# Performance work log

Measured on AMD Instinct MI355X. Metric: run time of the kernel, lower is better.

Reference implementation:

```python
import math
import jax, jax.numpy as jnp
import numpy as np

B, K, D, R = 8192, 64, 128, 8
EPSILON = 1.0  # alpha_scale, used as diffusion epsilon


def setup_inputs() -> dict:
    key = jax.random.key(0)
    k1, k2, k3 = jax.random.split(key, 3)
    y = jax.random.normal(k1, (B, D), dtype=jnp.float32)
    m = 0.2 * jax.random.normal(k2, (K, D), dtype=jnp.float32)          # init_mean_scale=0.2
    delta = jnp.full((K, D), -2.0, dtype=jnp.float32)                    # init_delta=-2.0
    U = 0.001 * jax.random.normal(k3, (K, D, R), dtype=jnp.float32)
    # log_alpha_raw = alpha_scale * log(ones(K)/K)
    log_alpha_raw = jnp.full((K,), math.log(1.0 / K), dtype=jnp.float32)
    return {"y": y, "m": m, "delta": delta, "U": U, "log_alpha_raw": log_alpha_raw}


def reference(y, m, delta, U, log_alpha_raw):
    """log z_theta(y) = logsumexp_k [log_alpha_k + log N(y; m_k, eps*S_k)],
    S_k = diag(exp(delta_k)) + U_k U_k^T, solved via Woodbury + Cholesky."""
    d = y.shape[-1]
    eps = jnp.asarray(EPSILON, y.dtype)
    log_alpha = (log_alpha_raw - jnp.mean(log_alpha_raw)) / EPSILON

    S_diag = jnp.exp(delta)            # [K, d]
    S_inv = 1.0 / S_diag               # [K, d]

    # Capacitance M_k = I_r + U_k^T diag(S_inv_k) U_k, Cholesky L_k
    V = S_inv[..., None] * U                              # [K, d, r]
    Mcap = jnp.eye(R, dtype=y.dtype) + jnp.einsum('kdr,kds->krs', U, V)  # [K, r, r]
    L = jnp.linalg.cholesky(Mcap)                         # [K, r, r]
    logdet_S = jnp.sum(jnp.log(S_diag), axis=-1) \
        + 2.0 * jnp.sum(jnp.log(jnp.diagonal(L, axis1=-2, axis2=-1)), axis=-1)  # [K]

    diff = y[:, None, :] - m[None, :, :]                  # [B, K, d]
    u1 = diff * S_inv[None]                               # [B, K, d]
    # Woodbury correction: solve M_k s = U_k^T u1 for all (b, k)
    t = jnp.einsum('kdr,bkd->krb', U, u1)                 # [K, r, B] (B as multiple RHS)
    z1 = jax.scipy.linalg.solve_triangular(L, t, lower=True)
    s = jax.scipy.linalg.solve_triangular(jnp.swapaxes(L, -1, -2), z1, lower=False)  # [K, r, B]
    Us = jnp.einsum('kdr,krb->bkd', U, s)                 # [B, K, d]
    S_inv_diff = u1 - Us * S_inv[None]                    # [B, K, d]

    quad = jnp.sum(diff * S_inv_diff, axis=-1)            # [B, K]
    log_norm = 0.5 * (d * (math.log(2.0 * math.pi) + jnp.log(eps)) + logdet_S)  # [K]
    logits = log_alpha[None, :] - 0.5 * quad / eps - log_norm[None, :]          # [B, K]
    return jax.scipy.special.logsumexp(logits, axis=-1)   # [B]
```

## Files before the change

kernel.cpp:

```cpp
#include <hip/hip_runtime.h>
#include <math.h>

#define D_DIM 128
#define K_DIM 64
#define R_DIM 8
#define B_DIM 8192
#define KG    4
#define KPB   16
#define ROWS  64
#define CHUNK 32
#define ENT   12

#define WS_TBL  0
#define WS_C0   (KG * D_DIM * KPB * ENT)
#define WS_PART (WS_C0 + K_DIM)

__global__ __launch_bounds__(128) void precomp_kernel(
    const float* __restrict__ m, const float* __restrict__ delta,
    const float* __restrict__ U, const float* __restrict__ lar,
    float* __restrict__ ws) {
  const int k = blockIdx.x;
  const int d = threadIdx.x;

  __shared__ float U_l[D_DIM][R_DIM];
  __shared__ float V_l[D_DIM][R_DIM];
  __shared__ float W_l[D_DIM][R_DIM];
  __shared__ float m_l[D_DIM];
  __shared__ float red[64];
  __shared__ float Linv_s[R_DIM][R_DIM];
  __shared__ float q_s[R_DIM];
  __shared__ float c0_s[1];
  __shared__ float redA[D_DIM], redB[D_DIM], redC[D_DIM];

  const float dl    = delta[k * D_DIM + d];
  const float s_inv = expf(-dl);
  const float mv    = m[k * D_DIM + d];
  m_l[d] = mv;
  const float* Up = U + (size_t)(k * D_DIM + d) * R_DIM;
#pragma unroll
  for (int r = 0; r < R_DIM; ++r) {
    float u = Up[r];
    U_l[d][r] = u;
    V_l[d][r] = u * s_inv;
  }
  redA[d] = dl;
  redB[d] = mv * mv * s_inv;
  redC[d] = (d < K_DIM) ? lar[d] : 0.f;
  __syncthreads();

  if (d < 64) {
    const int r = d >> 3, s = d & 7;
    float acc = (r == s) ? 1.0f : 0.0f;
#pragma unroll 8
    for (int dd = 0; dd < D_DIM; ++dd) acc += U_l[dd][r] * V_l[dd][s];
    red[d] = acc;
  }
  __syncthreads();

  for (int off = 64; off > 0; off >>= 1) {
    if (d < off) {
      redA[d] += redA[d + off];
      redB[d] += redB[d + off];
      redC[d] += redC[d + off];
    }
    __syncthreads();
  }

  if (d == 0) {
    float Lm[8][8];
#pragma unroll
    for (int i = 0; i < 8; ++i) {
#pragma unroll
      for (int j = 0; j < 8; ++j) {
        if (j > i) continue;
        float sum = red[i * 8 + j];
#pragma unroll
        for (int p = 0; p < 8; ++p)
          if (p < j) sum -= Lm[i][p] * Lm[j][p];
        if (i == j) Lm[i][i] = sqrtf(sum);
        else        Lm[i][j] = sum / Lm[j][j];
      }
    }
    float ld = 0.f;
#pragma unroll
    for (int i = 0; i < 8; ++i) ld += logf(Lm[i][i]);

    float Li[8][8];
#pragma unroll
    for (int i = 0; i < 8; ++i)
#pragma unroll
      for (int j = 0; j < 8; ++j) Li[i][j] = 0.f;
#pragma unroll
    for (int j = 0; j < 8; ++j) {
      Li[j][j] = 1.0f / Lm[j][j];
#pragma unroll
      for (int i = 0; i < 8; ++i) {
        if (i <= j) continue;
        float sum = 0.f;
#pragma unroll
        for (int p = 0; p < 8; ++p)
          if (p >= j && p < i) sum += Lm[i][p] * Li[p][j];
        Li[i][j] = -sum / Lm[i][i];
      }
    }
#pragma unroll
    for (int i = 0; i < 8; ++i)
#pragma unroll
      for (int j = 0; j < 8; ++j) Linv_s[i][j] = Li[i][j];

    const float mean = redC[0] * (1.0f / K_DIM);
    const float log_alpha = lar[k] - mean;
    const float logdetS = redA[0] + 2.0f * ld;
    const float LOG2PI = 1.8378770664093453f;
    const float log_norm = 0.5f * ((float)D_DIM * LOG2PI + logdetS);
    c0_s[0] = log_alpha - log_norm - 0.5f * redB[0];
  }
  __syncthreads();

  float Wr[R_DIM];
#pragma unroll
  for (int r = 0; r < R_DIM; ++r) {
    float acc = 0.f;
#pragma unroll
    for (int s2 = 0; s2 < R_DIM; ++s2)
      if (s2 <= r) acc += V_l[d][s2] * Linv_s[r][s2];
    Wr[r] = acc;
    W_l[d][r] = acc;
  }
  __syncthreads();

  if (d < R_DIM) {
    float acc = 0.f;
#pragma unroll 8
    for (int dd = 0; dd < D_DIM; ++dd) acc += W_l[dd][d] * m_l[dd];
    q_s[d] = acc;
  }
  __syncthreads();

  float hp = mv * s_inv;
#pragma unroll
  for (int r = 0; r < R_DIM; ++r) hp -= q_s[r] * Wr[r];

  float* e = ws + WS_TBL +
             (size_t)(((k >> 4) * D_DIM + d) * KPB + (k & 15)) * ENT;
#pragma unroll
  for (int r = 0; r < R_DIM; ++r) e[r] = Wr[r];
  e[8]  = -0.5f * s_inv;
  e[9]  = hp;
  e[10] = 0.f;
  e[11] = 0.f;

  if (d == 0) {
    float qq = 0.f;
#pragma unroll
    for (int r = 0; r < R_DIM; ++r) qq += q_s[r] * q_s[r];
    ws[WS_C0 + k] = c0_s[0] + 0.5f * qq;
  }
}

__global__ __launch_bounds__(512, 4) void logz_main(
    const float* __restrict__ y, const float* __restrict__ ws,
    float* __restrict__ part) {
  __shared__ float sT[CHUNK * KPB * ENT];
  __shared__ float sY[ROWS * 36];
  __shared__ float vals[ROWS * 17];

  const int tid  = threadIdx.x;
  const int lane = tid & 63;
  const int wv   = tid >> 6;
  const int rt   = (int)blockIdx.x >> 2;
  const int kg   = (int)blockIdx.x & 3;
  const int ki   = lane & 15;
  const int bi   = lane >> 4;
  const int rowA = wv * 8 + bi;
  const int rowB = rowA + 4;
  const int r0   = rt * ROWS;

  const float* __restrict__ tblG = ws + WS_TBL + (size_t)kg * (D_DIM * KPB * ENT);

  float gA = 0.f, gB = 0.f;
  float pA[8], pB[8];
#pragma unroll
  for (int r = 0; r < 8; ++r) { pA[r] = 0.f; pB[r] = 0.f; }

  const int yrow = tid >> 3, yseg = tid & 7;

  for (int c = 0; c < D_DIM / CHUNK; ++c) {
    __syncthreads();
    {
      const float* src = tblG + (size_t)c * (CHUNK * KPB * ENT);
#pragma unroll
      for (int j = 0; j < 3; ++j) {
        const int off = (wv * 3 + j) * 256;
        __builtin_amdgcn_global_load_lds(
            (const __attribute__((address_space(1))) void*)(src + off + lane * 4),
            (__attribute__((address_space(3))) void*)(sT + off),
            16, 0, 0);
      }
    }
    {
      const float4 v = *(const float4*)(y + (size_t)(r0 + yrow) * D_DIM
                                          + c * CHUNK + yseg * 4);
      *(float4*)(sY + yrow * 36 + yseg * 4) = v;
    }
    __syncthreads();
#pragma unroll
    for (int d4 = 0; d4 < CHUNK / 4; ++d4) {
      const float4 ya4 = *(const float4*)(sY + rowA * 36 + d4 * 4);
      const float4 yb4 = *(const float4*)(sY + rowB * 36 + d4 * 4);
#pragma unroll
      for (int j = 0; j < 4; ++j) {
        const float* e = sT + ((d4 * 4 + j) * KPB + ki) * ENT;
        const float4 w0 = *(const float4*)(e);
        const float4 w1 = *(const float4*)(e + 4);
        const float2 sh = *(const float2*)(e + 8);
        const float ya = (j == 0) ? ya4.x : (j == 1) ? ya4.y : (j == 2) ? ya4.z : ya4.w;
        const float yb = (j == 0) ? yb4.x : (j == 1) ? yb4.y : (j == 2) ? yb4.z : yb4.w;
        gA = fmaf(ya, fmaf(sh.x, ya, sh.y), gA);
        gB = fmaf(yb, fmaf(sh.x, yb, sh.y), gB);
        pA[0] = fmaf(ya, w0.x, pA[0]);  pB[0] = fmaf(yb, w0.x, pB[0]);
        pA[1] = fmaf(ya, w0.y, pA[1]);  pB[1] = fmaf(yb, w0.y, pB[1]);
        pA[2] = fmaf(ya, w0.z, pA[2]);  pB[2] = fmaf(yb, w0.z, pB[2]);
        pA[3] = fmaf(ya, w0.w, pA[3]);  pB[3] = fmaf(yb, w0.w, pB[3]);
        pA[4] = fmaf(ya, w1.x, pA[4]);  pB[4] = fmaf(yb, w1.x, pB[4]);
        pA[5] = fmaf(ya, w1.y, pA[5]);  pB[5] = fmaf(yb, w1.y, pB[5]);
        pA[6] = fmaf(ya, w1.z, pA[6]);  pB[6] = fmaf(yb, w1.z, pB[6]);
        pA[7] = fmaf(ya, w1.w, pA[7]);  pB[7] = fmaf(yb, w1.w, pB[7]);
      }
    }
  }

  const float cv = ws[WS_C0 + kg * KPB + ki];
  float qa = pA[0]*pA[0] + pA[1]*pA[1] + pA[2]*pA[2] + pA[3]*pA[3]
           + pA[4]*pA[4] + pA[5]*pA[5] + pA[6]*pA[6] + pA[7]*pA[7];
  float qb = pB[0]*pB[0] + pB[1]*pB[1] + pB[2]*pB[2] + pB[3]*pB[3]
           + pB[4]*pB[4] + pB[5]*pB[5] + pB[6]*pB[6] + pB[7]*pB[7];
  const float vA = cv + gA + 0.5f * qa;
  const float vB = cv + gB + 0.5f * qb;

  vals[rowA * 17 + ki] = vA;
  vals[rowB * 17 + ki] = vB;
  __syncthreads();

  if (tid < 64) {
    float mx = -INFINITY;
#pragma unroll
    for (int j = 0; j < KPB; ++j) mx = fmaxf(mx, vals[tid * 17 + j]);
    float s = 0.f;
#pragma unroll
    for (int j = 0; j < KPB; ++j) s += expf(vals[tid * 17 + j] - mx);
    *(float2*)(part + ((size_t)(r0 + tid) * KG + kg) * 2) = make_float2(mx, s);
  }
}

__global__ __launch_bounds__(256) void reduce_kernel(
    const float* __restrict__ part, float* __restrict__ out) {
  const int b = blockIdx.x * 256 + threadIdx.x;
  const float4 a0 = ((const float4*)part)[b * 2];
  const float4 a1 = ((const float4*)part)[b * 2 + 1];
  float mx = fmaxf(fmaxf(a0.x, a0.z), fmaxf(a1.x, a1.z));
  float s = a0.y * expf(a0.x - mx) + a0.w * expf(a0.z - mx)
          + a1.y * expf(a1.x - mx) + a1.w * expf(a1.z - mx);
  out[b] = mx + logf(s);
}

extern "C" void kernel_launch(void* const* d_in, const int* in_sizes, int n_in,
                              void* d_out, int out_size, void* d_ws, size_t ws_size,
                              hipStream_t stream) {
  const float* y     = (const float*)d_in[0];
  const float* m     = (const float*)d_in[1];
  const float* delta = (const float*)d_in[2];
  const float* U     = (const float*)d_in[3];
  const float* lar   = (const float*)d_in[4];
  float* out = (float*)d_out;
  float* ws  = (float*)d_ws;

  precomp_kernel<<<K_DIM, 128, 0, stream>>>(m, delta, U, lar, ws);
  logz_main<<<(B_DIM / ROWS) * KG, 512, 0, stream>>>(y, ws, ws + WS_PART);
  reduce_kernel<<<B_DIM / 256, 256, 0, stream>>>(ws + WS_PART, out);
}
```

Before: 94.73 us.

## Map one mixture component per wavefront with wave-uniform table loads

Reorganizes the main kernel so each of 16 wavefronts handles one component k and each lane handles one row, with 1024 threads per block. The per-component table is stored contiguously per k and read with wave-uniform (readfirstlane) addresses, which lets it go through scalar loads instead of being staged into LDS. The 64 rows of y are loaded into LDS once with an XOR swizzle to avoid bank conflicts, and the chunked load/sync loop is removed. The risk is that the larger block and the launch_bounds(1024, 8) hint may increase register pressure, and scalar-load latency is now on the inner loop.

```diff
diff --git a/kernel.cpp b/kernel.cpp
--- a/kernel.cpp
+++ b/kernel.cpp
@@ -8,11 +8,10 @@
 #define KG    4
 #define KPB   16
 #define ROWS  64
-#define CHUNK 32
 #define ENT   12
 
 #define WS_TBL  0
-#define WS_C0   (KG * D_DIM * KPB * ENT)
+#define WS_C0   (K_DIM * D_DIM * ENT)
 #define WS_PART (WS_C0 + K_DIM)
 
 __global__ __launch_bounds__(128) void precomp_kernel(
@@ -141,8 +140,7 @@
 #pragma unroll
   for (int r = 0; r < R_DIM; ++r) hp -= q_s[r] * Wr[r];
 
-  float* e = ws + WS_TBL +
-             (size_t)(((k >> 4) * D_DIM + d) * KPB + (k & 15)) * ENT;
+  float* e = ws + WS_TBL + ((size_t)k * D_DIM + d) * ENT;
 #pragma unroll
   for (int r = 0; r < R_DIM; ++r) e[r] = Wr[r];
   e[8]  = -0.5f * s_inv;
@@ -158,97 +156,80 @@
   }
 }
 
-__global__ __launch_bounds__(512, 4) void logz_main(
+__global__ __launch_bounds__(1024, 8) void logz_main(
     const float* __restrict__ y, const float* __restrict__ ws,
     float* __restrict__ part) {
-  __shared__ float sT[CHUNK * KPB * ENT];
-  __shared__ float sY[ROWS * 36];
-  __shared__ float vals[ROWS * 17];
+  __shared__ float4 sY[ROWS * 32];
+  __shared__ float vals[ROWS * (KPB + 1)];
 
   const int tid  = threadIdx.x;
   const int lane = tid & 63;
   const int wv   = tid >> 6;
   const int rt   = (int)blockIdx.x >> 2;
   const int kg   = (int)blockIdx.x & 3;
-  const int ki   = lane & 15;
-  const int bi   = lane >> 4;
-  const int rowA = wv * 8 + bi;
-  const int rowB = rowA + 4;
   const int r0   = rt * ROWS;
 
-  const float* __restrict__ tblG = ws + WS_TBL + (size_t)kg * (D_DIM * KPB * ENT);
-
-  float gA = 0.f, gB = 0.f;
-  float pA[8], pB[8];
-#pragma unroll
-  for (int r = 0; r < 8; ++r) { pA[r] = 0.f; pB[r] = 0.f; }
-
-  const int yrow = tid >> 3, yseg = tid & 7;
-
-  for (int c = 0; c < D_DIM / CHUNK; ++c) {
-    __syncthreads();
-    {
-      const float* src = tblG + (size_t)c * (CHUNK * KPB * ENT);
-#pragma unroll
-      for (int j = 0; j < 3; ++j) {
-        const int off = (wv * 3 + j) * 256;
-        __builtin_amdgcn_global_load_lds(
-            (const __attribute__((address_space(1))) void*)(src + off + lane * 4),
-            (__attribute__((address_space(3))) void*)(sT + off),
-            16, 0, 0);
-      }
-    }
-    {
-      const float4 v = *(const float4*)(y + (size_t)(r0 + yrow) * D_DIM
-                                          + c * CHUNK + yseg * 4);
-      *(float4*)(sY + yrow * 36 + yseg * 4) = v;
-    }
-    __syncthreads();
-#pragma unroll
-    for (int d4 = 0; d4 < CHUNK / 4; ++d4) {
-      const float4 ya4 = *(const float4*)(sY + rowA * 36 + d4 * 4);
-      const float4 yb4 = *(const float4*)(sY + rowB * 36 + d4 * 4);
-#pragma unroll
-      for (int j = 0; j < 4; ++j) {
-        const float* e = sT + ((d4 * 4 + j) * KPB + ki) * ENT;
-        const float4 w0 = *(const float4*)(e);
-        const float4 w1 = *(const float4*)(e + 4);
-        const float2 sh = *(const float2*)(e + 8);
-        const float ya = (j == 0) ? ya4.x : (j == 1) ? ya4.y : (j == 2) ? ya4.z : ya4.w;
-        const float yb = (j == 0) ? yb4.x : (j == 1) ? yb4.y : (j == 2) ? yb4.z : yb4.w;
-        gA = fmaf(ya, fmaf(sh.x, ya, sh.y), gA);
-        gB = fmaf(yb, fmaf(sh.x, yb, sh.y), gB);
-        pA[0] = fmaf(ya, w0.x, pA[0]);  pB[0] = fmaf(yb, w0.x, pB[0]);
-        pA[1] = fmaf(ya, w0.y, pA[1]);  pB[1] = fmaf(yb, w0.y, pB[1]);
-        pA[2] = fmaf(ya, w0.z, pA[2]);  pB[2] = fmaf(yb, w0.z, pB[2]);
-        pA[3] = fmaf(ya, w0.w, pA[3]);  pB[3] = fmaf(yb, w0.w, pB[3]);
-        pA[4] = fmaf(ya, w1.x, pA[4]);  pB[4] = fmaf(yb, w1.x, pB[4]);
-        pA[5] = fmaf(ya, w1.y, pA[5]);  pB[5] = fmaf(yb, w1.y, pB[5]);
-        pA[6] = fmaf(ya, w1.z, pA[6]);  pB[6] = fmaf(yb, w1.z, pB[6]);
-        pA[7] = fmaf(ya, w1.w, pA[7]);  pB[7] = fmaf(yb, w1.w, pB[7]);
-      }
-    }
-  }
-
-  const float cv = ws[WS_C0 + kg * KPB + ki];
-  float qa = pA[0]*pA[0] + pA[1]*pA[1] + pA[2]*pA[2] + pA[3]*pA[3]
-           + pA[4]*pA[4] + pA[5]*pA[5] + pA[6]*pA[6] + pA[7]*pA[7];
-  float qb = pB[0]*pB[0] + pB[1]*pB[1] + pB[2]*pB[2] + pB[3]*pB[3]
-           + pB[4]*pB[4] + pB[5]*pB[5] + pB[6]*pB[6] + pB[7]*pB[7];
-  const float vA = cv + gA + 0.5f * qa;
-  const float vB = cv + gB + 0.5f * qb;
-
-  vals[rowA * 17 + ki] = vA;
-  vals[rowB * 17 + ki] = vB;
+  {
+    const float4* ysrc = (const float4*)(y + (size_t)r0 * D_DIM);
+#pragma unroll
+    for (int j = 0; j < 2; ++j) {
+      const int i   = tid + j * 1024;
+      const int row = i >> 5, seg = i & 31;
+      sY[row * 32 + (seg ^ (row & 7))] = ysrc[i];
+    }
+  }
+  __syncthreads();
+
+  const int k   = kg * KPB + wv;
+  const int k_u = __builtin_amdgcn_readfirstlane(k);
+  const float*  t  = ws + WS_TBL + (size_t)k_u * (D_DIM * ENT);
+  const float4* t4 = (const float4*)t;
+  const float2* t2 = (const float2*)t;
+
+  const int swz = lane & 7;
+  const float4* yrow = sY + lane * 32;
+
+  float g = 0.f;
+  float p0 = 0.f, p1 = 0.f, p2 = 0.f, p3 = 0.f;
+  float p4 = 0.f, p5 = 0.f, p6 = 0.f, p7 = 0.f;
+
+#pragma unroll 4
+  for (int d4 = 0; d4 < D_DIM / 4; ++d4) {
+    const float4 yv = yrow[d4 ^ swz];
+#pragma unroll
+    for (int j = 0; j < 4; ++j) {
+      const int d = d4 * 4 + j;
+      const float4 w0 = t4[d * 3];
+      const float4 w1 = t4[d * 3 + 1];
+      const float2 sh = t2[d * 6 + 4];
+      const float yd = (j == 0) ? yv.x : (j == 1) ? yv.y : (j == 2) ? yv.z : yv.w;
+      g  = fmaf(yd, fmaf(sh.x, yd, sh.y), g);
+      p0 = fmaf(yd, w0.x, p0);
+      p1 = fmaf(yd, w0.y, p1);
+      p2 = fmaf(yd, w0.z, p2);
+      p3 = fmaf(yd, w0.w, p3);
+      p4 = fmaf(yd, w1.x, p4);
+      p5 = fmaf(yd, w1.y, p5);
+      p6 = fmaf(yd, w1.z, p6);
+      p7 = fmaf(yd, w1.w, p7);
+    }
+  }
+
+  const float cv = ws[WS_C0 + k_u];
+  const float qq = p0*p0 + p1*p1 + p2*p2 + p3*p3
+                 + p4*p4 + p5*p5 + p6*p6 + p7*p7;
+  const float val = cv + g + 0.5f * qq;
+
+  vals[lane * (KPB + 1) + wv] = val;
   __syncthreads();
 
   if (tid < 64) {
     float mx = -INFINITY;
 #pragma unroll
-    for (int j = 0; j < KPB; ++j) mx = fmaxf(mx, vals[tid * 17 + j]);
+    for (int j = 0; j < KPB; ++j) mx = fmaxf(mx, vals[tid * (KPB + 1) + j]);
     float s = 0.f;
 #pragma unroll
-    for (int j = 0; j < KPB; ++j) s += expf(vals[tid * 17 + j] - mx);
+    for (int j = 0; j < KPB; ++j) s += expf(vals[tid * (KPB + 1) + j] - mx);
     *(float2*)(part + ((size_t)(r0 + tid) * KG + kg) * 2) = make_float2(mx, s);
   }
 }
@@ -276,6 +257,6 @@
   float* ws  = (float*)d_ws;
 
   precomp_kernel<<<K_DIM, 128, 0, stream>>>(m, delta, U, lar, ws);
-  logz_main<<<(B_DIM / ROWS) * KG, 512, 0, stream>>>(y, ws, ws + WS_PART);
+  logz_main<<<(B_DIM / ROWS) * KG, 1024, 0, stream>>>(y, ws, ws + WS_PART);
   reduce_kernel<<<B_DIM / 256, 256, 0, stream>>>(ws + WS_PART, out);
 }
```

Measured after the change: 103.6 us. 1.09x slower.

## Register-block four rows per thread and preload the whole y tile into LDS

Applied to the files above, without the earlier changes.

The main kernel now uses 256 threads per block, with each thread accumulating four batch rows instead of two. This reuses every LDS table entry load across more rows and halves the table traffic per FMA. The full 64x128 y tile is loaded into padded LDS once up front instead of one chunk per iteration. The W entries are prescaled by 1/sqrt2 in precompute so the 0.5 multiply on the squared projection can be dropped. In exchange each thread holds more registers, each block has fewer waves, and LDS use per block grows.

```diff
diff --git a/kernel.cpp b/kernel.cpp
--- a/kernel.cpp
+++ b/kernel.cpp
@@ -8,6 +8,7 @@
 #define KG    4
 #define KPB   16
 #define ROWS  64
+#define RPT   4
 #define CHUNK 32
 #define ENT   12
 
@@ -141,10 +142,11 @@
 #pragma unroll
   for (int r = 0; r < R_DIM; ++r) hp -= q_s[r] * Wr[r];
 
+  const float INV_SQRT2 = 0.70710678118654752f;
   float* e = ws + WS_TBL +
              (size_t)(((k >> 4) * D_DIM + d) * KPB + (k & 15)) * ENT;
 #pragma unroll
-  for (int r = 0; r < R_DIM; ++r) e[r] = Wr[r];
+  for (int r = 0; r < R_DIM; ++r) e[r] = Wr[r] * INV_SQRT2;
   e[8]  = -0.5f * s_inv;
   e[9]  = hp;
   e[10] = 0.f;
@@ -158,97 +160,105 @@
   }
 }
 
-__global__ __launch_bounds__(512, 4) void logz_main(
+__global__ __launch_bounds__(256, 2) void logz_main(
     const float* __restrict__ y, const float* __restrict__ ws,
     float* __restrict__ part) {
-  __shared__ float sT[CHUNK * KPB * ENT];
-  __shared__ float sY[ROWS * 36];
-  __shared__ float vals[ROWS * 17];
+  __shared__ float4 sY4[ROWS * 33];
+  __shared__ float  sT[CHUNK * KPB * ENT];
+  __shared__ float  vals[ROWS * (KPB + 1)];
 
   const int tid  = threadIdx.x;
   const int lane = tid & 63;
   const int wv   = tid >> 6;
+  const int ki   = lane & 15;
+  const int bi   = lane >> 4;
   const int rt   = (int)blockIdx.x >> 2;
   const int kg   = (int)blockIdx.x & 3;
-  const int ki   = lane & 15;
-  const int bi   = lane >> 4;
-  const int rowA = wv * 8 + bi;
-  const int rowB = rowA + 4;
   const int r0   = rt * ROWS;
+  const int rowb = wv * 16 + bi;
+
+  {
+    const float4* ysrc = (const float4*)(y + (size_t)r0 * D_DIM);
+#pragma unroll
+    for (int j = 0; j < 8; ++j) {
+      const int idx = tid + j * 256;
+      sY4[(idx >> 5) * 33 + (idx & 31)] = ysrc[idx];
+    }
+  }
 
   const float* __restrict__ tblG = ws + WS_TBL + (size_t)kg * (D_DIM * KPB * ENT);
 
-  float gA = 0.f, gB = 0.f;
-  float pA[8], pB[8];
-#pragma unroll
-  for (int r = 0; r < 8; ++r) { pA[r] = 0.f; pB[r] = 0.f; }
-
-  const int yrow = tid >> 3, yseg = tid & 7;
+  float g[RPT];
+  float p[RPT][8];
+#pragma unroll
+  for (int j = 0; j < RPT; ++j) {
+    g[j] = 0.f;
+#pragma unroll
+    for (int r = 0; r < 8; ++r) p[j][r] = 0.f;
+  }
 
   for (int c = 0; c < D_DIM / CHUNK; ++c) {
     __syncthreads();
     {
       const float* src = tblG + (size_t)c * (CHUNK * KPB * ENT);
 #pragma unroll
-      for (int j = 0; j < 3; ++j) {
-        const int off = (wv * 3 + j) * 256;
+      for (int j = 0; j < 6; ++j) {
+        const int off = (wv * 6 + j) * 256;
         __builtin_amdgcn_global_load_lds(
             (const __attribute__((address_space(1))) void*)(src + off + lane * 4),
             (__attribute__((address_space(3))) void*)(sT + off),
             16, 0, 0);
       }
     }
-    {
-      const float4 v = *(const float4*)(y + (size_t)(r0 + yrow) * D_DIM
-                                          + c * CHUNK + yseg * 4);
-      *(float4*)(sY + yrow * 36 + yseg * 4) = v;
-    }
     __syncthreads();
+
 #pragma unroll
     for (int d4 = 0; d4 < CHUNK / 4; ++d4) {
-      const float4 ya4 = *(const float4*)(sY + rowA * 36 + d4 * 4);
-      const float4 yb4 = *(const float4*)(sY + rowB * 36 + d4 * 4);
-#pragma unroll
-      for (int j = 0; j < 4; ++j) {
-        const float* e = sT + ((d4 * 4 + j) * KPB + ki) * ENT;
+      float4 yv[RPT];
+#pragma unroll
+      for (int j = 0; j < RPT; ++j)
+        yv[j] = sY4[(rowb + 4 * j) * 33 + c * (CHUNK / 4) + d4];
+#pragma unroll
+      for (int dj = 0; dj < 4; ++dj) {
+        const float* e = sT + ((d4 * 4 + dj) * KPB + ki) * ENT;
         const float4 w0 = *(const float4*)(e);
         const float4 w1 = *(const float4*)(e + 4);
         const float2 sh = *(const float2*)(e + 8);
-        const float ya = (j == 0) ? ya4.x : (j == 1) ? ya4.y : (j == 2) ? ya4.z : ya4.w;
-        const float yb = (j == 0) ? yb4.x : (j == 1) ? yb4.y : (j == 2) ? yb4.z : yb4.w;
-        gA = fmaf(ya, fmaf(sh.x, ya, sh.y), gA);
-        gB = fmaf(yb, fmaf(sh.x, yb, sh.y), gB);
-        pA[0] = fmaf(ya, w0.x, pA[0]);  pB[0] = fmaf(yb, w0.x, pB[0]);
-        pA[1] = fmaf(ya, w0.y, pA[1]);  pB[1] = fmaf(yb, w0.y, pB[1]);
-        pA[2] = fmaf(ya, w0.z, pA[2]);  pB[2] = fmaf(yb, w0.z, pB[2]);
-        pA[3] = fmaf(ya, w0.w, pA[3]);  pB[3] = fmaf(yb, w0.w, pB[3]);
-        pA[4] = fmaf(ya, w1.x, pA[4]);  pB[4] = fmaf(yb, w1.x, pB[4]);
-        pA[5] = fmaf(ya, w1.y, pA[5]);  pB[5] = fmaf(yb, w1.y, pB[5]);
-        pA[6] = fmaf(ya, w1.z, pA[6]);  pB[6] = fmaf(yb, w1.z, pB[6]);
-        pA[7] = fmaf(ya, w1.w, pA[7]);  pB[7] = fmaf(yb, w1.w, pB[7]);
+#pragma unroll
+        for (int j = 0; j < RPT; ++j) {
+          const float yd = (dj == 0) ? yv[j].x : (dj == 1) ? yv[j].y
+                         : (dj == 2) ? yv[j].z : yv[j].w;
+          g[j]    = fmaf(yd, fmaf(sh.x, yd, sh.y), g[j]);
+          p[j][0] = fmaf(yd, w0.x, p[j][0]);
+          p[j][1] = fmaf(yd, w0.y, p[j][1]);
+          p[j][2] = fmaf(yd, w0.z, p[j][2]);
+          p[j][3] = fmaf(yd, w0.w, p[j][3]);
+          p[j][4] = fmaf(yd, w1.x, p[j][4]);
+          p[j][5] = fmaf(yd, w1.y, p[j][5]);
+          p[j][6] = fmaf(yd, w1.z, p[j][6]);
+          p[j][7] = fmaf(yd, w1.w, p[j][7]);
+        }
       }
     }
   }
 
   const float cv = ws[WS_C0 + kg * KPB + ki];
-  float qa = pA[0]*pA[0] + pA[1]*pA[1] + pA[2]*pA[2] + pA[3]*pA[3]
-           + pA[4]*pA[4] + pA[5]*pA[5] + pA[6]*pA[6] + pA[7]*pA[7];
-  float qb = pB[0]*pB[0] + pB[1]*pB[1] + pB[2]*pB[2] + pB[3]*pB[3]
-           + pB[4]*pB[4] + pB[5]*pB[5] + pB[6]*pB[6] + pB[7]*pB[7];
-  const float vA = cv + gA + 0.5f * qa;
-  const float vB = cv + gB + 0.5f * qb;
-
-  vals[rowA * 17 + ki] = vA;
-  vals[rowB * 17 + ki] = vB;
+#pragma unroll
+  for (int j = 0; j < RPT; ++j) {
+    const float qq = p[j][0]*p[j][0] + p[j][1]*p[j][1] + p[j][2]*p[j][2]
+                   + p[j][3]*p[j][3] + p[j][4]*p[j][4] + p[j][5]*p[j][5]
+                   + p[j][6]*p[j][6] + p[j][7]*p[j][7];
+    vals[(rowb + 4 * j) * (KPB + 1) + ki] = cv + g[j] + qq;
+  }
   __syncthreads();
 
   if (tid < 64) {
     float mx = -INFINITY;
 #pragma unroll
-    for (int j = 0; j < KPB; ++j) mx = fmaxf(mx, vals[tid * 17 + j]);
+    for (int j = 0; j < KPB; ++j) mx = fmaxf(mx, vals[tid * (KPB + 1) + j]);
     float s = 0.f;
 #pragma unroll
-    for (int j = 0; j < KPB; ++j) s += expf(vals[tid * 17 + j] - mx);
+    for (int j = 0; j < KPB; ++j) s += expf(vals[tid * (KPB + 1) + j] - mx);
     *(float2*)(part + ((size_t)(r0 + tid) * KG + kg) * 2) = make_float2(mx, s);
   }
 }
@@ -276,6 +286,6 @@
   float* ws  = (float*)d_ws;
 
   precomp_kernel<<<K_DIM, 128, 0, stream>>>(m, delta, U, lar, ws);
-  logz_main<<<(B_DIM / ROWS) * KG, 512, 0, stream>>>(y, ws, ws + WS_PART);
+  logz_main<<<(B_DIM / ROWS) * KG, 256, 0, stream>>>(y, ws, ws + WS_PART);
   reduce_kernel<<<B_DIM / 256, 256, 0, stream>>>(ws + WS_PART, out);
 }
```

Result: slower. 100.3 us (+5.9%).
